# Performance work log

Measured on AMD Instinct MI355X. Metric: run time of the kernel, lower is better.

## Reference

```python
import jax, jax.numpy as jnp
import numpy as np
from jax import lax


def _conv2d_same(x, w):
    # x: [B,Cin,H,W], w: [Cout,Cin,kh,kw], stride 1, SAME padding
    return lax.conv_general_dilated(x, w, (1, 1), 'SAME',
                                    dimension_numbers=('NCHW', 'OIHW', 'NCHW'))


def _descriptor(f_flat, w_a, b_a, w_aa, b_aa, w_m, b_m, w_mm, b_mm):
    # f_flat: [B,C,HW]; channel MLPs on avg/max pooled descriptors (1x1 convs == linear)
    avg = jnp.mean(f_flat, axis=-1)  # [B,C]
    mx = jnp.max(f_flat, axis=-1)    # [B,C]
    a = jax.nn.relu(avg @ w_a.T + b_a) @ w_aa.T + b_aa  # [B,C]
    m = jax.nn.relu(mx @ w_m.T + b_m) @ w_mm.T + b_mm   # [B,C]
    return a + m


def _spatial_gate(a_flat, b, c, h, w, conv1_w, conv1_b, conv2_w, conv2_b):
    a = a_flat.reshape(b, c, h, w)
    pooled = jnp.stack([jnp.mean(a, axis=1), jnp.max(a, axis=1)], axis=1)  # [B,2,H,W]
    y = jax.nn.relu(_conv2d_same(pooled, conv1_w) + conv1_b[None, :, None, None])
    y = _conv2d_same(y, conv2_w) + conv2_b[None, :, None, None]
    return jax.nn.softmax(y.reshape(b, 1, h * w), axis=-1)  # [B,1,HW]


def _cafm_forward(f1, f2,
                  w_avg1, b_avg1, w_max1, b_max1, w_avg11, b_avg11, w_max11, b_max11,
                  w_avg2, b_avg2, w_max2, b_max2, w_avg22, b_avg22, w_max22, b_max22,
                  conv1_w, conv1_b, conv2_w, conv2_b):
    b, c, h, w = f1.shape
    f1f = f1.reshape(b, c, h * w)
    f2f = f2.reshape(b, c, h * w)
    a1 = _descriptor(f1f, w_avg1, b_avg1, w_avg11, b_avg11, w_max1, b_max1, w_max11, b_max11)
    a2 = _descriptor(f2f, w_avg2, b_avg2, w_avg22, b_avg22, w_max2, b_max2, w_max22, b_max22)
    cross = jnp.einsum('bi,bj->bij', a1, a2)  # [B,C,C]
    at1 = jnp.einsum('bij,bjn->bin', jax.nn.softmax(cross, axis=-1), f1f)
    at2 = jnp.einsum('bij,bjn->bin', jax.nn.softmax(cross.transpose(0, 2, 1), axis=-1), f2f)
    g1 = _spatial_gate(at1, b, c, h, w, conv1_w, conv1_b, conv2_w, conv2_b)
    g2 = _spatial_gate(at2, b, c, h, w, conv1_w, conv1_b, conv2_w, conv2_b)
    o1 = (f1f * g1 + f1f).reshape(b, c, h, w)
    o2 = (f2f * g2 + f2f).reshape(b, c, h, w)
    return o1, o2


def setup_inputs() -> dict:
    key = jax.random.key(0)
    ks = jax.random.split(key, 24)
    B, C, H, W = 4, 64, 256, 256
    CR = 32  # reduction channels
    s = 0.05
    d = {
        'f1': jax.random.normal(ks[0], (B, C, H, W), jnp.float32),
        'f2': jax.random.normal(ks[1], (B, C, H, W), jnp.float32),
        'w_avg1': jax.random.normal(ks[2], (CR, C), jnp.float32) * s,
        'b_avg1': jnp.zeros((CR,), jnp.float32),
        'w_max1': jax.random.normal(ks[3], (CR, C), jnp.float32) * s,
        'b_max1': jnp.zeros((CR,), jnp.float32),
        'w_avg11': jax.random.normal(ks[4], (C, CR), jnp.float32) * s,
        'b_avg11': jnp.zeros((C,), jnp.float32),
        'w_max11': jax.random.normal(ks[5], (C, CR), jnp.float32) * s,
        'b_max11': jnp.zeros((C,), jnp.float32),
        'w_avg2': jax.random.normal(ks[6], (CR, C), jnp.float32) * s,
        'b_avg2': jnp.zeros((CR,), jnp.float32),
        'w_max2': jax.random.normal(ks[7], (CR, C), jnp.float32) * s,
        'b_max2': jnp.zeros((CR,), jnp.float32),
        'w_avg22': jax.random.normal(ks[8], (C, CR), jnp.float32) * s,
        'b_avg22': jnp.zeros((C,), jnp.float32),
        'w_max22': jax.random.normal(ks[9], (C, CR), jnp.float32) * s,
        'b_max22': jnp.zeros((C,), jnp.float32),
        'conv1_w': jax.random.normal(ks[10], (1, 2, 3, 3), jnp.float32) * s,
        'conv1_b': jnp.zeros((1,), jnp.float32),
        'conv2_w': jax.random.normal(ks[11], (1, 1, 3, 3), jnp.float32) * s,
        'conv2_b': jnp.zeros((1,), jnp.float32),
    }
    return d


def reference(f1, f2,
              w_avg1, b_avg1, w_max1, b_max1, w_avg11, b_avg11, w_max11, b_max11,
              w_avg2, b_avg2, w_max2, b_max2, w_avg22, b_avg22, w_max22, b_max22,
              conv1_w, conv1_b, conv2_w, conv2_b):
    return _cafm_forward(f1, f2,
                         w_avg1, b_avg1, w_max1, b_max1, w_avg11, b_avg11, w_max11, b_max11,
                         w_avg2, b_avg2, w_max2, b_max2, w_avg22, b_avg22, w_max22, b_max22,
                         conv1_w, conv1_b, conv2_w, conv2_b)
```

## Files before the change

### kernel.cpp

```cpp
#include <hip/hip_runtime.h>
#include <hip/hip_bf16.h>
#include <cstdint>

#define HW 65536

typedef __attribute__((ext_vector_type(8))) short bf16x8;
typedef __attribute__((ext_vector_type(4))) float f32x4;

#define D0   0
#define D1A  4096
#define D1   4608
#define D2   4624
#define D3   8720
#define FLAGS_BYTES 51264
#define OFF_PARTS 12816
#define OFF_PARTM 143888
#define OFF_AVG   274960
#define OFF_MXA   275472
#define OFF_PB    275984
#define OFF_POOL  292368
#define OFF_BM    1340944
#define OFF_BS    1341968
#define OFF_Y     1342992

__device__ __forceinline__ unsigned short f2bf(float x) {
  union { float f; unsigned u; } v; v.f = x;
  unsigned r = v.u + 0x7fffu + ((v.u >> 16) & 1u);
  return (unsigned short)(r >> 16);
}

__device__ __forceinline__ void st_wt_f32(float* p, float v) {
  __hip_atomic_store(p, v, __ATOMIC_RELAXED, __HIP_MEMORY_SCOPE_AGENT);
}
__device__ __forceinline__ void st_wt_u32(unsigned* p, unsigned v) {
  __hip_atomic_store(p, v, __ATOMIC_RELAXED, __HIP_MEMORY_SCOPE_AGENT);
}

__device__ __forceinline__ void signal(unsigned* slot) {
  __syncthreads();
  if (threadIdx.x == 0) {
    asm volatile("s_waitcnt vmcnt(0)" ::: "memory");
    st_wt_u32(slot, 1u);
  }
}

__device__ __forceinline__ void wait_slots(const unsigned* fl, int idx, bool active) {
  bool ok;
  do {
    ok = true;
    if (active)
      ok = (__hip_atomic_load(fl + idx, __ATOMIC_RELAXED, __HIP_MEMORY_SCOPE_AGENT) != 0u);
    if (!ok) __builtin_amdgcn_s_sleep(8);
  } while (__syncthreads_and((int)ok) == 0);
  asm volatile("" ::: "memory");
}

__device__ __forceinline__ void stage_tile(const float* __restrict__ fb, int n0,
                                           unsigned short* tile, int tid) {
  int r0 = tid >> 6, cb = (tid & 63) << 2;
#pragma unroll 4
  for (int i = 0; i < 16; ++i) {
    int row = (i << 2) + r0;
    float4 v = *(const float4*)(fb + (size_t)row * HW + n0 + cb);
    __hip_bfloat162 lo = __float22bfloat162_rn(make_float2(v.x, v.y));
    __hip_bfloat162 hi = __float22bfloat162_rn(make_float2(v.z, v.w));
    unsigned* d = (unsigned*)(tile + row * 258 + cb);
    d[0] = *(unsigned*)&lo;
    d[1] = *(unsigned*)&hi;
  }
}

template <bool STORE>
__device__ __forceinline__ void p0_tile(const float* __restrict__ fb, int n0, int ssp,
                                        int chunk, unsigned short* tile,
                                        float* __restrict__ ws, int lane, int wv) {
  int ls = lane >> 4, lp = lane & 15;
#pragma unroll
  for (int rg = 0; rg < 4; ++rg) {
    int row = (wv << 4) + (rg << 2) + ls;
    const float4* rp = (const float4*)(fb + (size_t)row * HW + n0);
    float sum = 0.f, mx = -3.4e38f;
#pragma unroll
    for (int i = 0; i < 4; ++i) {
      int j = lp + (i << 4);
      float4 v = rp[j];
      sum += (v.x + v.y) + (v.z + v.w);
      mx = fmaxf(mx, fmaxf(fmaxf(v.x, v.y), fmaxf(v.z, v.w)));
      if (STORE) {
        __hip_bfloat162 lo = __float22bfloat162_rn(make_float2(v.x, v.y));
        __hip_bfloat162 hi = __float22bfloat162_rn(make_float2(v.z, v.w));
        unsigned* d = (unsigned*)(tile + row * 258 + (j << 2));
        d[0] = *(unsigned*)&lo;
        d[1] = *(unsigned*)&hi;
      }
    }
#pragma unroll
    for (int o = 1; o < 16; o <<= 1) {
      sum += __shfl_xor(sum, o);
      mx = fmaxf(mx, __shfl_xor(mx, o));
    }
    if (lp == 0) {
      st_wt_f32(ws + OFF_PARTS + (((ssp << 6) + row) << 8) + chunk, sum);
      st_wt_f32(ws + OFF_PARTM + (((ssp << 6) + row) << 8) + chunk, mx);
    }
  }
}

__global__ __launch_bounds__(256, 4) void k_mega(
    const float* __restrict__ f1, const float* __restrict__ f2,
    float* __restrict__ ws, float* __restrict__ out,
    const float* __restrict__ w_avg1, const float* __restrict__ b_avg1,
    const float* __restrict__ w_max1, const float* __restrict__ b_max1,
    const float* __restrict__ w_avg11, const float* __restrict__ b_avg11,
    const float* __restrict__ w_max11, const float* __restrict__ b_max11,
    const float* __restrict__ w_avg2, const float* __restrict__ b_avg2,
    const float* __restrict__ w_max2, const float* __restrict__ b_max2,
    const float* __restrict__ w_avg22, const float* __restrict__ b_avg22,
    const float* __restrict__ w_max22, const float* __restrict__ b_max22,
    const float* __restrict__ cw1, const float* __restrict__ cb1,
    const float* __restrict__ cw2, const float* __restrict__ cb2) {

  __shared__ union {
    unsigned short tile[64 * 258];
    struct { float pl[2][20][36]; float t1l[18][34]; } cv;
    struct { float avg1[64], mx1[64], avg2[64], mx2[64],
             ha1[32], hm1[32], ha2[32], hm2[32],
             a1[64], a2[64], mm[4]; } mlp;
    float yst[512];
  } sm;
  __shared__ float red[8];

  unsigned* fl = (unsigned*)ws;
  const int tid = threadIdx.x;
  const int bx  = blockIdx.x;
  const int lane = tid & 63, wv = tid >> 6;

  const int ss1 = bx >> 8, chunk = bx & 255, n0 = chunk << 8;
  const float* fb1 = f1 + ((size_t)ss1 << 22);
  const float* fb2 = f2 + ((size_t)ss1 << 22);

  p0_tile<true >(fb1, n0, ss1,     chunk, sm.tile, ws, lane, wv);
  p0_tile<false>(fb2, n0, ss1 + 4, chunk, sm.tile, ws, lane, wv);
  signal(fl + D0 + (bx << 2));

  if (bx < 128) {
    int ssx = bx >> 4;
    wait_slots(fl, D0 + ((((ssx & 3) << 8) | tid) << 2), true);
    int r = (bx << 2) + wv;
    float4 s4 = *(const float4*)(ws + OFF_PARTS + (r << 8) + (lane << 2));
    float4 m4 = *(const float4*)(ws + OFF_PARTM + (r << 8) + (lane << 2));
    float s = (s4.x + s4.y) + (s4.z + s4.w);
    float m = fmaxf(fmaxf(m4.x, m4.y), fmaxf(m4.z, m4.w));
    for (int o = 32; o > 0; o >>= 1) {
      s += __shfl_xor(s, o);
      m = fmaxf(m, __shfl_xor(m, o));
    }
    if (lane == 0) {
      st_wt_f32(ws + OFF_AVG + r, s * (1.f / 65536.f));
      st_wt_f32(ws + OFF_MXA + r, m);
    }
    signal(fl + D1A + (bx << 2));
  }

  if (bx < 4) {
    int b = bx;
    {
      int fidx = (tid < 16) ? (b * 16 + tid) : ((b + 4) * 16 + (tid - 16));
      wait_slots(fl, D1A + (fidx << 2), tid < 32);
    }
    if (tid < 64) {
      sm.mlp.avg1[tid] = ws[OFF_AVG + (b << 6) + tid];
      sm.mlp.mx1[tid]  = ws[OFF_MXA + (b << 6) + tid];
      sm.mlp.avg2[tid] = ws[OFF_AVG + ((b + 4) << 6) + tid];
      sm.mlp.mx2[tid]  = ws[OFF_MXA + ((b + 4) << 6) + tid];
    }
    __syncthreads();
    if (tid < 32) {
      float s1 = b_avg1[tid], s2 = b_max1[tid], s3 = b_avg2[tid], s4 = b_max2[tid];
      for (int c = 0; c < 64; ++c) {
        s1 += w_avg1[tid * 64 + c] * sm.mlp.avg1[c];
        s2 += w_max1[tid * 64 + c] * sm.mlp.mx1[c];
        s3 += w_avg2[tid * 64 + c] * sm.mlp.avg2[c];
        s4 += w_max2[tid * 64 + c] * sm.mlp.mx2[c];
      }
      sm.mlp.ha1[tid] = fmaxf(s1, 0.f); sm.mlp.hm1[tid] = fmaxf(s2, 0.f);
      sm.mlp.ha2[tid] = fmaxf(s3, 0.f); sm.mlp.hm2[tid] = fmaxf(s4, 0.f);
    }
    __syncthreads();
    if (tid < 64) {
      float s1 = b_avg11[tid] + b_max11[tid];
      float s2 = b_avg22[tid] + b_max22[tid];
      for (int k = 0; k < 32; ++k) {
        s1 += w_avg11[tid * 32 + k] * sm.mlp.ha1[k] + w_max11[tid * 32 + k] * sm.mlp.hm1[k];
        s2 += w_avg22[tid * 32 + k] * sm.mlp.ha2[k] + w_max22[tid * 32 + k] * sm.mlp.hm2[k];
      }
      sm.mlp.a1[tid] = s1; sm.mlp.a2[tid] = s2;
    }
    __syncthreads();
    if (wv == 0) {
      float v = sm.mlp.a2[lane], mxv = v, mnv = v;
      for (int o = 32; o > 0; o >>= 1) {
        mxv = fmaxf(mxv, __shfl_xor(mxv, o));
        mnv = fminf(mnv, __shfl_xor(mnv, o));
      }
      if (lane == 0) { sm.mlp.mm[0] = mxv; sm.mlp.mm[1] = mnv; }
    } else if (wv == 1) {
      float v = sm.mlp.a1[lane], mxv = v, mnv = v;
      for (int o = 32; o > 0; o >>= 1) {
        mxv = fmaxf(mxv, __shfl_xor(mxv, o));
        mnv = fminf(mnv, __shfl_xor(mnv, o));
      }
      if (lane == 0) { sm.mlp.mm[2] = mxv; sm.mlp.mm[3] = mnv; }
    }
    __syncthreads();
    if (tid < 128) {
      int i = tid & 63;
      bool first = tid < 64;
      float s = first ? sm.mlp.a1[i] : sm.mlp.a2[i];
      const float* col = first ? sm.mlp.a2 : sm.mlp.a1;
      float m = (s >= 0.f) ? s * (first ? sm.mlp.mm[0] : sm.mlp.mm[2])
                           : s * (first ? sm.mlp.mm[1] : sm.mlp.mm[3]);
      float sum = 0.f;
      for (int j = 0; j < 64; ++j) sum += __expf(s * col[j] - m);
      float inv = 1.f / sum;
      int ssl = first ? b : (4 + b);
      unsigned* rowp = (unsigned*)(ws + OFF_PB) + (ssl << 11) + (i << 5);
      for (int jj = 0; jj < 32; ++jj) {
        unsigned lo = f2bf(__expf(s * col[2 * jj] - m) * inv);
        unsigned hi = f2bf(__expf(s * col[2 * jj + 1] - m) * inv);
        st_wt_u32(rowp + jj, lo | (hi << 16));
      }
    }
    signal(fl + D1 + (b << 2));
  }

  wait_slots(fl, D1 + (ss1 << 2), tid == 0);

  {
    const unsigned short* Pb16 = (const unsigned short*)(ws + OFF_PB);
    const int c = lane & 15, q = lane >> 4;
    const int pxb = wv << 6;

    auto mfma_tile = [&](int ss) {
      bf16x8 A[4][2];
      const unsigned short* Prow = Pb16 + (ss << 12);
#pragma unroll
      for (int mt = 0; mt < 4; ++mt)
#pragma unroll
        for (int s = 0; s < 2; ++s)
          A[mt][s] = *(const bf16x8*)(Prow + ((mt * 16 + c) << 6) + s * 32 + q * 8);
      float* poolp = ws + OFF_POOL + (size_t)ss * (2 * HW);
#pragma unroll
      for (int nt = 0; nt < 4; ++nt) {
        int pcol = pxb + (nt << 4) + c;
        union { bf16x8 v; unsigned short s[8]; } u0, u1;
#pragma unroll
        for (int j = 0; j < 8; ++j) {
          u0.s[j] = sm.tile[(q * 8 + j) * 258 + pcol];
          u1.s[j] = sm.tile[(32 + q * 8 + j) * 258 + pcol];
        }
        f32x4 acc[4];
#pragma unroll
        for (int mt = 0; mt < 4; ++mt) {
          acc[mt] = (f32x4){0.f, 0.f, 0.f, 0.f};
          acc[mt] = __builtin_amdgcn_mfma_f32_16x16x32_bf16(A[mt][0], u0.v, acc[mt], 0, 0, 0);
          acc[mt] = __builtin_amdgcn_mfma_f32_16x16x32_bf16(A[mt][1], u1.v, acc[mt], 0, 0, 0);
        }
        float sum = 0.f, mxv = -3.4e38f;
#pragma unroll
        for (int mt = 0; mt < 4; ++mt)
#pragma unroll
          for (int r = 0; r < 4; ++r) {
            float v = acc[mt][r];
            sum += v;
            mxv = fmaxf(mxv, v);
          }
        sum += __shfl_xor(sum, 16);
        sum += __shfl_xor(sum, 32);
        mxv = fmaxf(mxv, __shfl_xor(mxv, 16));
        mxv = fmaxf(mxv, __shfl_xor(mxv, 32));
        int px = n0 + pcol;
        if (q == 0) st_wt_f32(poolp + px, sum * (1.f / 64.f));
        if (q == 1) st_wt_f32(poolp + HW + px, mxv);
      }
    };

    if (bx < 4) {
      __syncthreads();
      stage_tile(fb1, n0, sm.tile, tid);
      __syncthreads();
    }
    mfma_tile(ss1);
    __syncthreads();
    stage_tile(fb2, n0, sm.tile, tid);
    __syncthreads();
    mfma_tile(ss1 + 4);
  }
  signal(fl + D2 + (bx << 2));

  {
    int ss = bx >> 7, tile_id = bx & 127;
    int h0 = (tile_id >> 3) << 4;
    int w0 = (tile_id & 7) << 5;
    {
      int rr = h0 - 2 + tid;
      bool act = (tid < 20) && (rr >= 0) && (rr < 256);
      wait_slots(fl, D2 + ((((ss & 3) << 8) + rr) << 2), act);
    }
    const float* pp = ws + OFF_POOL + (size_t)ss * (2 * HW);
    float c1b = cb1[0], c2b = cb2[0];
    for (int i = tid; i < 1440; i += 256) {
      int ch = (i >= 720), rem = i - ch * 720;
      int rr = rem / 36, cc = rem - rr * 36;
      int h = h0 - 2 + rr, w = w0 - 2 + cc;
      float v = 0.f;
      if (h >= 0 && h < 256 && w >= 0 && w < 256) v = pp[ch * HW + (h << 8) + w];
      sm.cv.pl[ch][rr][cc] = v;
    }
    __syncthreads();
    for (int i = tid; i < 612; i += 256) {
      int rr = i / 34, cc = i - rr * 34;
      int h = h0 - 1 + rr, w = w0 - 1 + cc;
      float s = c1b;
#pragma unroll
      for (int ci = 0; ci < 2; ++ci)
#pragma unroll
        for (int kh = 0; kh < 3; ++kh)
#pragma unroll
          for (int kw = 0; kw < 3; ++kw)
            s += sm.cv.pl[ci][rr + kh][cc + kw] * cw1[ci * 9 + kh * 3 + kw];
      bool in = (h >= 0 && h < 256 && w >= 0 && w < 256);
      sm.cv.t1l[rr][cc] = in ? fmaxf(s, 0.f) : 0.f;
    }
    __syncthreads();
    float myy[2];
    float m = -3.4e38f;
#pragma unroll
    for (int k2 = 0; k2 < 2; ++k2) {
      int i = tid + (k2 << 8);
      int rr = i >> 5, cc = i & 31;
      float s = c2b;
#pragma unroll
      for (int kh = 0; kh < 3; ++kh)
#pragma unroll
        for (int kw = 0; kw < 3; ++kw)
          s += sm.cv.t1l[rr + kh][cc + kw] * cw2[kh * 3 + kw];
      st_wt_f32(ws + OFF_Y + (ss << 16) + ((h0 + rr) << 8) + w0 + cc, s);
      myy[k2] = s;
      m = fmaxf(m, s);
    }
    for (int o = 32; o > 0; o >>= 1) m = fmaxf(m, __shfl_xor(m, o));
    if (lane == 0) red[wv] = m;
    __syncthreads();
    float Mb = fmaxf(fmaxf(red[0], red[1]), fmaxf(red[2], red[3]));
    float z = __expf(myy[0] - Mb) + __expf(myy[1] - Mb);
    for (int o = 32; o > 0; o >>= 1) z += __shfl_xor(z, o);
    if (lane == 0) red[4 + wv] = z;
    __syncthreads();
    if (tid == 0) {
      st_wt_f32(ws + OFF_BM + bx, Mb);
      st_wt_f32(ws + OFF_BS + bx, red[4] + red[5] + red[6] + red[7]);
    }
  }
  signal(fl + D3 + (bx << 2));

  {
    int ss = bx >> 7, wq = bx & 127;
    wait_slots(fl, D3 + ((ss * 128 + (tid & 127)) << 2), tid < 128);
    float m = (tid < 128) ? ws[OFF_BM + ss * 128 + tid] : -3.4e38f;
    for (int o = 32; o > 0; o >>= 1) m = fmaxf(m, __shfl_xor(m, o));
    if (lane == 0) red[wv] = m;
    __syncthreads();
    float M = fmaxf(fmaxf(red[0], red[1]), fmaxf(red[2], red[3]));
    float z = (tid < 128) ? __expf(ws[OFF_BM + ss * 128 + tid] - M) * ws[OFF_BS + ss * 128 + tid] : 0.f;
    for (int o = 32; o > 0; o >>= 1) z += __shfl_xor(z, o);
    if (lane == 0) red[4 + wv] = z;
    __syncthreads();
    float iZ = 1.f / (red[4] + red[5] + red[6] + red[7]);
    int p0 = wq << 9;
    if (tid < 128) {
      float4 vy = *(const float4*)(ws + OFF_Y + (ss << 16) + p0 + (tid << 2));
      *(float4*)(&sm.yst[tid << 2]) = vy;
    }
    __syncthreads();
    const float* fsl = (ss >= 4) ? (f2 + ((size_t)(ss - 4) << 22))
                                 : (f1 + ((size_t)ss << 22));
    float* osl = out + ((size_t)ss << 22);
    int c0 = tid >> 7;
    int pxo = (tid & 127) << 2;
    float4 yv = *(const float4*)(&sm.yst[pxo]);
    float4 g;
    g.x = 1.f + __expf(yv.x - M) * iZ;
    g.y = 1.f + __expf(yv.y - M) * iZ;
    g.z = 1.f + __expf(yv.z - M) * iZ;
    g.w = 1.f + __expf(yv.w - M) * iZ;
#pragma unroll 8
    for (int i = 0; i < 32; ++i) {
      int ch = (i << 1) + c0;
      size_t gi = (size_t)ch * HW + p0 + pxo;
      float4 fv = *(const float4*)(fsl + gi);
      float4 o;
      o.x = fv.x * g.x; o.y = fv.y * g.y; o.z = fv.z * g.z; o.w = fv.w * g.w;
      *(float4*)(osl + gi) = o;
    }
  }
}

extern "C" void kernel_launch(void* const* d_in, const int* in_sizes, int n_in,
                              void* d_out, int out_size, void* d_ws, size_t ws_size,
                              hipStream_t stream) {
  const float* f1 = (const float*)d_in[0];
  const float* f2 = (const float*)d_in[1];
  const float* w_avg1  = (const float*)d_in[2];
  const float* b_avg1  = (const float*)d_in[3];
  const float* w_max1  = (const float*)d_in[4];
  const float* b_max1  = (const float*)d_in[5];
  const float* w_avg11 = (const float*)d_in[6];
  const float* b_avg11 = (const float*)d_in[7];
  const float* w_max11 = (const float*)d_in[8];
  const float* b_max11 = (const float*)d_in[9];
  const float* w_avg2  = (const float*)d_in[10];
  const float* b_avg2  = (const float*)d_in[11];
  const float* w_max2  = (const float*)d_in[12];
  const float* b_max2  = (const float*)d_in[13];
  const float* w_avg22 = (const float*)d_in[14];
  const float* b_avg22 = (const float*)d_in[15];
  const float* w_max22 = (const float*)d_in[16];
  const float* b_max22 = (const float*)d_in[17];
  const float* conv1_w = (const float*)d_in[18];
  const float* conv1_b = (const float*)d_in[19];
  const float* conv2_w = (const float*)d_in[20];
  const float* conv2_b = (const float*)d_in[21];
  float* ws = (float*)d_ws;
  float* out = (float*)d_out;

  hipMemsetAsync(d_ws, 0, FLAGS_BYTES, stream);
  k_mega<<<1024, 256, 0, stream>>>(f1, f2, ws, out,
                                   w_avg1, b_avg1, w_max1, b_max1,
                                   w_avg11, b_avg11, w_max11, b_max11,
                                   w_avg2, b_avg2, w_max2, b_max2,
                                   w_avg22, b_avg22, w_max22, b_max22,
                                   conv1_w, conv1_b, conv2_w, conv2_b);
}
```

Measured before the change: 343.5 us.

## Compute channel MLP and softmax redundantly per block, removing cross-block barrier

Every block now recomputes the tiny descriptor MLPs and the cross-attention softmax row statistics itself, then builds the bf16 A fragments for the MFMA in registers. This removes the four-block MLP stage, its global P buffer and the D1 flag wait that every block previously spun on, along with the extra tile restaging in blocks 0-3. The cost is redundant MLP and exp work in all 1024 blocks plus extra shared memory. The final output writes also switch to nontemporal stores.

```diff
diff --git a/kernel.cpp b/kernel.cpp
--- a/kernel.cpp
+++ b/kernel.cpp
@@ -9,7 +9,6 @@
 
 #define D0   0
 #define D1A  4096
-#define D1   4608
 #define D2   4624
 #define D3   8720
 #define FLAGS_BYTES 51264
@@ -17,17 +16,10 @@
 #define OFF_PARTM 143888
 #define OFF_AVG   274960
 #define OFF_MXA   275472
-#define OFF_PB    275984
 #define OFF_POOL  292368
 #define OFF_BM    1340944
 #define OFF_BS    1341968
 #define OFF_Y     1342992
-
-__device__ __forceinline__ unsigned short f2bf(float x) {
-  union { float f; unsigned u; } v; v.f = x;
-  unsigned r = v.u + 0x7fffu + ((v.u >> 16) & 1u);
-  return (unsigned short)(r >> 16);
-}
 
 __device__ __forceinline__ void st_wt_f32(float* p, float v) {
   __hip_atomic_store(p, v, __ATOMIC_RELAXED, __HIP_MEMORY_SCOPE_AGENT);
@@ -123,12 +115,13 @@
   __shared__ union {
     unsigned short tile[64 * 258];
     struct { float pl[2][20][36]; float t1l[18][34]; } cv;
-    struct { float avg1[64], mx1[64], avg2[64], mx2[64],
-             ha1[32], hm1[32], ha2[32], hm2[32],
-             a1[64], a2[64], mm[4]; } mlp;
     float yst[512];
   } sm;
   __shared__ float red[8];
+  __shared__ float s_in[4][64];
+  __shared__ float s_h[4][32];
+  __shared__ float s_a1[64], s_a2[64], s_mm[4];
+  __shared__ float s_rm[2][64], s_ri[2][64];
 
   unsigned* fl = (unsigned*)ws;
   const int tid = threadIdx.x;
@@ -162,93 +155,97 @@
     signal(fl + D1A + (bx << 2));
   }
 
-  if (bx < 4) {
-    int b = bx;
-    {
-      int fidx = (tid < 16) ? (b * 16 + tid) : ((b + 4) * 16 + (tid - 16));
-      wait_slots(fl, D1A + (fidx << 2), tid < 32);
-    }
-    if (tid < 64) {
-      sm.mlp.avg1[tid] = ws[OFF_AVG + (b << 6) + tid];
-      sm.mlp.mx1[tid]  = ws[OFF_MXA + (b << 6) + tid];
-      sm.mlp.avg2[tid] = ws[OFF_AVG + ((b + 4) << 6) + tid];
-      sm.mlp.mx2[tid]  = ws[OFF_MXA + ((b + 4) << 6) + tid];
-    }
-    __syncthreads();
-    if (tid < 32) {
-      float s1 = b_avg1[tid], s2 = b_max1[tid], s3 = b_avg2[tid], s4 = b_max2[tid];
-      for (int c = 0; c < 64; ++c) {
-        s1 += w_avg1[tid * 64 + c] * sm.mlp.avg1[c];
-        s2 += w_max1[tid * 64 + c] * sm.mlp.mx1[c];
-        s3 += w_avg2[tid * 64 + c] * sm.mlp.avg2[c];
-        s4 += w_max2[tid * 64 + c] * sm.mlp.mx2[c];
-      }
-      sm.mlp.ha1[tid] = fmaxf(s1, 0.f); sm.mlp.hm1[tid] = fmaxf(s2, 0.f);
-      sm.mlp.ha2[tid] = fmaxf(s3, 0.f); sm.mlp.hm2[tid] = fmaxf(s4, 0.f);
-    }
-    __syncthreads();
-    if (tid < 64) {
-      float s1 = b_avg11[tid] + b_max11[tid];
-      float s2 = b_avg22[tid] + b_max22[tid];
-      for (int k = 0; k < 32; ++k) {
-        s1 += w_avg11[tid * 32 + k] * sm.mlp.ha1[k] + w_max11[tid * 32 + k] * sm.mlp.hm1[k];
-        s2 += w_avg22[tid * 32 + k] * sm.mlp.ha2[k] + w_max22[tid * 32 + k] * sm.mlp.hm2[k];
-      }
-      sm.mlp.a1[tid] = s1; sm.mlp.a2[tid] = s2;
-    }
-    __syncthreads();
-    if (wv == 0) {
-      float v = sm.mlp.a2[lane], mxv = v, mnv = v;
-      for (int o = 32; o > 0; o >>= 1) {
-        mxv = fmaxf(mxv, __shfl_xor(mxv, o));
-        mnv = fminf(mnv, __shfl_xor(mnv, o));
-      }
-      if (lane == 0) { sm.mlp.mm[0] = mxv; sm.mlp.mm[1] = mnv; }
-    } else if (wv == 1) {
-      float v = sm.mlp.a1[lane], mxv = v, mnv = v;
-      for (int o = 32; o > 0; o >>= 1) {
-        mxv = fmaxf(mxv, __shfl_xor(mxv, o));
-        mnv = fminf(mnv, __shfl_xor(mnv, o));
-      }
-      if (lane == 0) { sm.mlp.mm[2] = mxv; sm.mlp.mm[3] = mnv; }
-    }
-    __syncthreads();
-    if (tid < 128) {
-      int i = tid & 63;
-      bool first = tid < 64;
-      float s = first ? sm.mlp.a1[i] : sm.mlp.a2[i];
-      const float* col = first ? sm.mlp.a2 : sm.mlp.a1;
-      float m = (s >= 0.f) ? s * (first ? sm.mlp.mm[0] : sm.mlp.mm[2])
-                           : s * (first ? sm.mlp.mm[1] : sm.mlp.mm[3]);
-      float sum = 0.f;
-      for (int j = 0; j < 64; ++j) sum += __expf(s * col[j] - m);
-      float inv = 1.f / sum;
-      int ssl = first ? b : (4 + b);
-      unsigned* rowp = (unsigned*)(ws + OFF_PB) + (ssl << 11) + (i << 5);
-      for (int jj = 0; jj < 32; ++jj) {
-        unsigned lo = f2bf(__expf(s * col[2 * jj] - m) * inv);
-        unsigned hi = f2bf(__expf(s * col[2 * jj + 1] - m) * inv);
-        st_wt_u32(rowp + jj, lo | (hi << 16));
-      }
-    }
-    signal(fl + D1 + (b << 2));
-  }
-
-  wait_slots(fl, D1 + (ss1 << 2), tid == 0);
-
   {
-    const unsigned short* Pb16 = (const unsigned short*)(ws + OFF_PB);
+    int fidx = (tid < 16) ? (ss1 * 16 + tid) : ((ss1 + 4) * 16 + (tid - 16));
+    wait_slots(fl, D1A + (fidx << 2), tid < 32);
+  }
+  if (tid < 64) {
+    s_in[0][tid] = ws[OFF_AVG + (ss1 << 6) + tid];
+    s_in[1][tid] = ws[OFF_MXA + (ss1 << 6) + tid];
+    s_in[2][tid] = ws[OFF_AVG + ((ss1 + 4) << 6) + tid];
+    s_in[3][tid] = ws[OFF_MXA + ((ss1 + 4) << 6) + tid];
+  }
+  __syncthreads();
+  if (tid < 128) {
+    int u = tid & 31, which = tid >> 5;
+    const float* W = (which == 0) ? w_avg1 : (which == 1) ? w_max1
+                   : (which == 2) ? w_avg2 : w_max2;
+    const float* B = (which == 0) ? b_avg1 : (which == 1) ? b_max1
+                   : (which == 2) ? b_avg2 : b_max2;
+    float s = B[u];
+    for (int c2 = 0; c2 < 64; ++c2) s += W[u * 64 + c2] * s_in[which][c2];
+    s_h[which][u] = fmaxf(s, 0.f);
+  }
+  __syncthreads();
+  if (tid < 128) {
+    int u = tid & 63, which = tid >> 6;
+    const float* Wa = which ? w_avg22 : w_avg11;
+    const float* Wm = which ? w_max22 : w_max11;
+    float s = which ? (b_avg22[u] + b_max22[u]) : (b_avg11[u] + b_max11[u]);
+    const float* ha = s_h[which ? 2 : 0];
+    const float* hm = s_h[which ? 3 : 1];
+    for (int k = 0; k < 32; ++k) s += Wa[u * 32 + k] * ha[k] + Wm[u * 32 + k] * hm[k];
+    (which ? s_a2 : s_a1)[u] = s;
+  }
+  __syncthreads();
+  if (wv == 0) {
+    float v = s_a2[lane], mxv = v, mnv = v;
+    for (int o = 32; o > 0; o >>= 1) {
+      mxv = fmaxf(mxv, __shfl_xor(mxv, o));
+      mnv = fminf(mnv, __shfl_xor(mnv, o));
+    }
+    if (lane == 0) { s_mm[0] = mxv; s_mm[1] = mnv; }
+  } else if (wv == 1) {
+    float v = s_a1[lane], mxv = v, mnv = v;
+    for (int o = 32; o > 0; o >>= 1) {
+      mxv = fmaxf(mxv, __shfl_xor(mxv, o));
+      mnv = fminf(mnv, __shfl_xor(mnv, o));
+    }
+    if (lane == 0) { s_mm[2] = mxv; s_mm[3] = mnv; }
+  }
+  __syncthreads();
+  {
+    int r = tid >> 1, half = tid & 1;
+    int sel = r >> 6, i = r & 63;
+    float sv = sel ? s_a2[i] : s_a1[i];
+    const float* col = sel ? s_a1 : s_a2;
+    float mrow = (sv >= 0.f) ? sv * (sel ? s_mm[2] : s_mm[0])
+                             : sv * (sel ? s_mm[3] : s_mm[1]);
+    float sum = 0.f;
+    int j0 = half << 5;
+    for (int j = j0; j < j0 + 32; ++j) sum += __expf(sv * col[j] - mrow);
+    sum += __shfl_xor(sum, 1);
+    if (half == 0) { s_rm[sel][i] = mrow; s_ri[sel][i] = 1.f / sum; }
+  }
+  __syncthreads();
+
+  {
     const int c = lane & 15, q = lane >> 4;
     const int pxb = wv << 6;
 
-    auto mfma_tile = [&](int ss) {
-      bf16x8 A[4][2];
-      const unsigned short* Prow = Pb16 + (ss << 12);
-#pragma unroll
-      for (int mt = 0; mt < 4; ++mt)
-#pragma unroll
-        for (int s = 0; s < 2; ++s)
-          A[mt][s] = *(const bf16x8*)(Prow + ((mt * 16 + c) << 6) + s * 32 + q * 8);
+    auto build_A = [&](int sel, bf16x8 (&A)[4][2]) {
+      const float* col = sel ? s_a1 : s_a2;
+#pragma unroll
+      for (int mt = 0; mt < 4; ++mt) {
+        int i = mt * 16 + c;
+        float sv = sel ? s_a2[i] : s_a1[i];
+        float mrow = s_rm[sel][i], inv = s_ri[sel][i];
+#pragma unroll
+        for (int s = 0; s < 2; ++s) {
+          union { bf16x8 v; __hip_bfloat162 h[4]; } u;
+#pragma unroll
+          for (int jj = 0; jj < 4; ++jj) {
+            int j = s * 32 + q * 8 + jj * 2;
+            float e0 = __expf(sv * col[j]     - mrow) * inv;
+            float e1 = __expf(sv * col[j + 1] - mrow) * inv;
+            u.h[jj] = __float22bfloat162_rn(make_float2(e0, e1));
+          }
+          A[mt][s] = u.v;
+        }
+      }
+    };
+
+    auto mfma_tile = [&](int ss, const bf16x8 (&A)[4][2]) {
       float* poolp = ws + OFF_POOL + (size_t)ss * (2 * HW);
 #pragma unroll
       for (int nt = 0; nt < 4; ++nt) {
@@ -285,16 +282,14 @@
       }
     };
 
-    if (bx < 4) {
-      __syncthreads();
-      stage_tile(fb1, n0, sm.tile, tid);
-      __syncthreads();
-    }
-    mfma_tile(ss1);
+    bf16x8 A[4][2];
+    build_A(0, A);
+    mfma_tile(ss1, A);
     __syncthreads();
     stage_tile(fb2, n0, sm.tile, tid);
     __syncthreads();
-    mfma_tile(ss1 + 4);
+    build_A(1, A);
+    mfma_tile(ss1 + 4, A);
   }
   signal(fl + D2 + (bx << 2));
 
@@ -389,7 +384,7 @@
     int c0 = tid >> 7;
     int pxo = (tid & 127) << 2;
     float4 yv = *(const float4*)(&sm.yst[pxo]);
-    float4 g;
+    f32x4 g;
     g.x = 1.f + __expf(yv.x - M) * iZ;
     g.y = 1.f + __expf(yv.y - M) * iZ;
     g.z = 1.f + __expf(yv.z - M) * iZ;
@@ -398,10 +393,9 @@
     for (int i = 0; i < 32; ++i) {
       int ch = (i << 1) + c0;
       size_t gi = (size_t)ch * HW + p0 + pxo;
-      float4 fv = *(const float4*)(fsl + gi);
-      float4 o;
-      o.x = fv.x * g.x; o.y = fv.y * g.y; o.z = fv.z * g.z; o.w = fv.w * g.w;
-      *(float4*)(osl + gi) = o;
+      f32x4 fv = *(const f32x4*)(fsl + gi);
+      f32x4 o = fv * g;
+      __builtin_nontemporal_store(o, (f32x4*)(osl + gi));
     }
   }
 }
@@ -434,7 +428,7 @@
   float* ws = (float*)d_ws;
   float* out = (float*)d_out;
 
-  hipMemsetAsync(d_ws, 0, FLAGS_BYTES, stream);
+  (void)hipMemsetAsync(d_ws, 0, FLAGS_BYTES, stream);
   k_mega<<<1024, 256, 0, stream>>>(f1, f2, ws, out,
                                    w_avg1, b_avg1, w_max1, b_max1,
                                    w_avg11, b_avg11, w_max11, b_max11,
```

New measurement: 326.0 us. 1.05x faster.
